# Optimization experiments

Measured on AMD Instinct MI355X. Metric: run time of the kernel, lower is better.

## Reference

```python
import jax, jax.numpy as jnp
import numpy as np

# module hyperparameters (init_kwargs)
WEIGHT = 2e-9
SIGMA_RGB = 0.15   # images in [0,1]; equals canonical 15/255
SIGMA_XY = 100.0
SCALE = 0.5

N, C, K, H, W = 4, 3, 21, 128, 128


def _nearest(x, oh, ow):
    """torch F.interpolate(mode='nearest'): src = floor(dst * in/out)."""
    h, w = x.shape[-2], x.shape[-1]
    iy = jnp.floor(jnp.arange(oh) * (h / oh)).astype(jnp.int32)
    ix = jnp.floor(jnp.arange(ow) * (w / ow)).astype(jnp.int32)
    return x[..., iy[:, None], ix[None, :]]


def _bilinear(x, oh, ow):
    """torch F.interpolate(mode='bilinear', align_corners=False)."""
    h, w = x.shape[-2], x.shape[-1]

    def coords(o, s):
        c = (jnp.arange(o, dtype=jnp.float32) + 0.5) * (s / o) - 0.5
        c = jnp.clip(c, 0.0, s - 1.0)
        c0 = jnp.floor(c).astype(jnp.int32)
        c1 = jnp.minimum(c0 + 1, s - 1)
        return c0, c1, c - c0

    y0, y1, wy = coords(oh, h)
    x0, x1, wx = coords(ow, w)
    wy = wy[:, None]
    wx = wx[None, :]
    v00 = x[..., y0[:, None], x0[None, :]]
    v01 = x[..., y0[:, None], x1[None, :]]
    v10 = x[..., y1[:, None], x0[None, :]]
    v11 = x[..., y1[:, None], x1[None, :]]
    top = v00 * (1.0 - wx) + v01 * wx
    bot = v10 * (1.0 - wx) + v11 * wx
    return top * (1.0 - wy) + bot * wy


def setup_inputs() -> dict:
    key = jax.random.key(0)
    k1, k2 = jax.random.split(key)
    images = jax.random.uniform(k1, (N, C, H, W), jnp.float32)
    segmentations = jax.random.uniform(k2, (N, K, H, W), jnp.float32)
    ROIs = jnp.ones((N, H, W), jnp.float32)
    return {"images": images, "segmentations": segmentations, "ROIs": ROIs}


def reference(images, segmentations, ROIs):
    oh, ow = int(H * SCALE), int(W * SCALE)
    img_s = _nearest(images, oh, ow)           # [N,3,oh,ow]
    seg_s = _bilinear(segmentations, oh, ow)   # [N,K,oh,ow]
    roi_s = _nearest(ROIs, oh, ow)             # [N,oh,ow]
    seg_m = seg_s * roi_s[:, None]             # seg * ROI (per class)
    sxy = SIGMA_XY * SCALE

    # exact dense Gaussian bilateral kernel that the permutohedral lattice
    # (bilateralfilter_batch) approximates: k(i,j) = exp(-|p_i-p_j|^2/(2 sxy^2)
    #                                                  -|I_i-I_j|^2/(2 srgb^2))
    yy, xx = jnp.meshgrid(jnp.arange(oh, dtype=jnp.float32),
                          jnp.arange(ow, dtype=jnp.float32), indexing="ij")
    pos = jnp.stack([xx, yy], 0) / sxy         # [2,oh,ow]

    def per_image(img, seg):
        feat = jnp.concatenate([pos, img / SIGMA_RGB], 0).reshape(5, -1).T  # [P,5]
        sq = jnp.sum(feat * feat, axis=-1)                                  # [P]
        d2 = jnp.maximum(sq[:, None] + sq[None, :] - 2.0 * (feat @ feat.T), 0.0)
        Wk = jnp.exp(-0.5 * d2)                                             # [P,P]
        s = seg.reshape(K, -1)                                              # [K,P]
        AS = s @ Wk                                                         # filtered seg
        return jnp.sum(s * AS)

    vals = jax.vmap(per_image)(img_s, seg_m)   # [N]
    loss = -(jnp.sum(vals)) / N                # densecrf_loss
    return WEIGHT * loss
```

## Files before the change

kernel.cpp:

```cpp
#include <hip/hip_runtime.h>

#define NIMG 4
#define CCH  3
#define KCH  21
#define HIN  128
#define WIN  128
#define OH   64
#define OW   64
#define PPX  (OH*OW)
#define NPIX (NIMG*PPX)

#define PRE2 1.20112241f

#define SEGW  24
#define FEATW 8

#define BLOCK  256
#define JCHUNK 256
#define IBLK   64

#define NSLOT  64

typedef _Float16 half_t;
typedef half_t half8  __attribute__((ext_vector_type(8)));
typedef float  f32x4v __attribute__((ext_vector_type(4)));

#define FEATH_OFF ((size_t)NPIX*SEGW*2)
#define SQF_OFF   (FEATH_OFF + (size_t)NPIX*FEATW*2)
#define SLOT_OFF  (SQF_OFF + (size_t)NPIX*4)

__global__ __launch_bounds__(BLOCK) void crf_prep(const float* __restrict__ img,
                                                  const float* __restrict__ seg,
                                                  const float* __restrict__ roi,
                                                  half_t* __restrict__ segH,
                                                  half_t* __restrict__ featH,
                                                  float* __restrict__ sqF,
                                                  float* __restrict__ slots) {
    int g  = blockIdx.x * BLOCK + threadIdx.x;
    int q  = g >> 14;
    int pl = g & (NPIX - 1);
    int n  = pl >> 12;
    int p  = pl & (PPX - 1);
    int y = p >> 6, x = p & 63;
    int y2 = 2 * y, x2 = 2 * x;

    if (q < SEGW) {
        float v = 0.0f;
        if (q < KCH) {
            const float* s0 = seg + (((size_t)n * KCH + q) * HIN + y2) * WIN + x2;
            float r = roi[((size_t)n * HIN + y2) * WIN + x2];
            v = 0.25f * (s0[0] + s0[1] + s0[WIN] + s0[WIN + 1]) * r;
        }
        segH[(size_t)pl * SEGW + q] = (half_t)v;
    } else if (q == 24) {
        float fx = (float)x * (PRE2 / 50.0f);
        float fy = (float)y * (PRE2 / 50.0f);
        const size_t ib = (((size_t)n * CCH) * HIN + y2) * WIN + x2;
        float fr = img[ib]                         * (PRE2 / 0.15f);
        float fg = img[ib + (size_t)HIN * WIN]     * (PRE2 / 0.15f);
        float fb = img[ib + 2 * (size_t)HIN * WIN] * (PRE2 / 0.15f);
        half_t h0 = (half_t)fx, h1 = (half_t)fy, h2 = (half_t)fr,
               h3 = (half_t)fg, h4 = (half_t)fb;
        half8 fh = {h0, h1, h2, h3, h4, (half_t)0, (half_t)0, (half_t)0};
        *(half8*)(featH + (size_t)pl * FEATW) = fh;
        float a0 = (float)h0, a1 = (float)h1, a2 = (float)h2,
              a3 = (float)h3, a4 = (float)h4;
        sqF[pl] = 0.5f * (a0 * a0 + a1 * a1 + a2 * a2 + a3 * a3 + a4 * a4);
    } else if (q == 25) {
        if (pl < NSLOT) slots[pl * 16] = 0.0f;
    }
}

__global__ __launch_bounds__(BLOCK, 8) void crf_main(const half_t* __restrict__ segH,
                                                     const half_t* __restrict__ featH,
                                                     const float* __restrict__ sqF,
                                                     float* __restrict__ slots) {
    const int bx = blockIdx.x;
    const int n  = blockIdx.y;

    int g = 0;
#pragma unroll
    for (int t = 1; t < 16; ++t) {
        int off = 64 * t - 2 * t * (t - 1);
        if (bx >= off) g = t;
    }
    int rem = bx - (64 * g - 2 * g * (g - 1));
    int c   = 16 - g;
    int iq  = (rem >= c) + (rem >= 2 * c) + (rem >= 3 * c);
    int I   = 4 * g + iq;
    int J   = g + (rem - iq * c);
    const bool diag = (J == (I >> 2));

    const half_t* segN  = segH  + (size_t)n * PPX * SEGW;
    const half_t* featN = featH + (size_t)n * PPX * FEATW;
    const float*  sqN   = sqF   + (size_t)n * PPX;

    __shared__ alignas(16) half_t segJ[JCHUNK * SEGW];
    __shared__ alignas(16) half_t featJ[JCHUNK * FEATW];
    __shared__ alignas(16) half_t zrow[8];
    __shared__ float hJ[JCHUNK];
    __shared__ float wsum[BLOCK / 64];

    const int tid  = threadIdx.x;
    const int lane = tid & 63, wv = tid >> 6;
    const int m = lane & 15, quad = lane >> 4;
    const int ih  = wv >> 1;
    const int jt0 = (wv & 1) * 8;
    const int ib0 = I * 4 + ih * 2;
    const int ib1 = ib0 + 1;
    const int i00 = ib0 << 4;
    const int i01 = i00 + 16;
    const int Jt  = J << 4;
    const int kq  = (quad < 2) ? quad : 2;

    half8 hz = {};

    half8 aseg0  = *(const half8*)(segN  + (size_t)(i00 + m) * SEGW + kq * 8);
    half8 aseg1  = *(const half8*)(segN  + (size_t)(i01 + m) * SEGW + kq * 8);
    half8 afeat0 = *(const half8*)(featN + (size_t)(i00 + m) * FEATW);
    half8 afeat1 = *(const half8*)(featN + (size_t)(i01 + m) * FEATW);
    f32x4v hi0   = *(const f32x4v*)(sqN + i00 + quad * 4);
    f32x4v hi1   = *(const f32x4v*)(sqN + i01 + quad * 4);
    if (quad == 3) { aseg0 = hz; aseg1 = hz; }
    if (quad != 0) { afeat0 = hz; afeat1 = hz; }
    f32x4v nh0 = -hi0, nh1 = -hi1;

    {
        const f32x4v* gsrc = (const f32x4v*)(segN + (size_t)((size_t)Jt << 4) * SEGW);
        f32x4v* ldst = (f32x4v*)segJ;
#pragma unroll
        for (int v = 0; v < 3; ++v) ldst[tid + v * BLOCK] = gsrc[tid + v * BLOCK];
        ((f32x4v*)featJ)[tid] = ((const f32x4v*)(featN + (size_t)((size_t)Jt << 4) * FEATW))[tid];
        hJ[tid] = sqN[(Jt << 4) + tid];
        if (tid < 8) zrow[tid] = (half_t)0;
    }
    __syncthreads();

    const half_t* bsp; int bstep;
    if (quad == 3) { bsp = zrow;                                    bstep = 0; }
    else           { bsp = segJ + (jt0 * 16 + m) * SEGW + quad * 8; bstep = 16 * SEGW; }
    const half_t* bfp; int fstep;
    if (quad == 0) { bfp = featJ + (jt0 * 16 + m) * FEATW;          fstep = 16 * FEATW; }
    else           { bfp = zrow;                                    fstep = 0; }

    float hcv[8];
#pragma unroll
    for (int t = 0; t < 8; ++t) hcv[t] = hJ[(jt0 + t) * 16 + m];

    float racc0 = 0.0f, racc1 = 0.0f;
    const f32x4v zero4 = {0.0f, 0.0f, 0.0f, 0.0f};

#pragma unroll
    for (int t = 0; t < 8; ++t) {
        half8 bseg = *(const half8*)(bsp + t * bstep);
        half8 bft  = *(const half8*)(bfp + t * fstep);
        const float hc = hcv[t];
        const int jb = Jt + jt0 + t;
        const int jg = (jb << 4) + m;

        if (!diag || jb >= ib0) {
            f32x4v c4 = {nh0[0] - hc, nh0[1] - hc, nh0[2] - hc, nh0[3] - hc};
            f32x4v E  = __builtin_amdgcn_mfma_f32_16x16x32_f16(afeat0, bft, c4, 0, 0, 0);
            f32x4v Gs = __builtin_amdgcn_mfma_f32_16x16x32_f16(aseg0, bseg, zero4, 0, 0, 0);
            if (!diag) {
#pragma unroll
                for (int r = 0; r < 4; ++r)
                    racc0 = fmaf(__builtin_amdgcn_exp2f(E[r]), Gs[r], racc0);
            } else if (jb > ib0) {
#pragma unroll
                for (int r = 0; r < 4; ++r)
                    racc0 = fmaf(__builtin_amdgcn_exp2f(E[r] + 1.0f), Gs[r], racc0);
            } else {
#pragma unroll
                for (int r = 0; r < 4; ++r) {
                    int ig = i00 + quad * 4 + r;
                    float sel = (jg > ig) ? 1.0f : ((jg == ig) ? 0.0f : -100000.0f);
                    racc0 = fmaf(__builtin_amdgcn_exp2f(E[r] + sel), Gs[r], racc0);
                }
            }
        }

        if (!diag || jb >= ib1) {
            f32x4v c4 = {nh1[0] - hc, nh1[1] - hc, nh1[2] - hc, nh1[3] - hc};
            f32x4v E  = __builtin_amdgcn_mfma_f32_16x16x32_f16(afeat1, bft, c4, 0, 0, 0);
            f32x4v Gs = __builtin_amdgcn_mfma_f32_16x16x32_f16(aseg1, bseg, zero4, 0, 0, 0);
            if (!diag) {
#pragma unroll
                for (int r = 0; r < 4; ++r)
                    racc1 = fmaf(__builtin_amdgcn_exp2f(E[r]), Gs[r], racc1);
            } else if (jb > ib1) {
#pragma unroll
                for (int r = 0; r < 4; ++r)
                    racc1 = fmaf(__builtin_amdgcn_exp2f(E[r] + 1.0f), Gs[r], racc1);
            } else {
#pragma unroll
                for (int r = 0; r < 4; ++r) {
                    int ig = i01 + quad * 4 + r;
                    float sel = (jg > ig) ? 1.0f : ((jg == ig) ? 0.0f : -100000.0f);
                    racc1 = fmaf(__builtin_amdgcn_exp2f(E[r] + sel), Gs[r], racc1);
                }
            }
        }
    }

    float racc = racc0 + racc1;
#pragma unroll
    for (int off = 32; off > 0; off >>= 1) racc += __shfl_down(racc, off);
    if (lane == 0) wsum[wv] = racc;
    __syncthreads();
    if (tid == 0) {
        float s = wsum[0] + wsum[1] + wsum[2] + wsum[3];
        if (!diag) s *= 2.0f;
        int slot = (bx + 544 * n) & (NSLOT - 1);
        atomicAdd(&slots[slot * 16], s);
    }
}

__global__ __launch_bounds__(64) void crf_final(const float* __restrict__ slots,
                                                float* __restrict__ out) {
    int lane = threadIdx.x;
    float v = slots[lane * 16];
#pragma unroll
    for (int off = 32; off > 0; off >>= 1) v += __shfl_down(v, off);
    if (lane == 0) out[0] = v * (-5.0e-10f);
}

extern "C" void kernel_launch(void* const* d_in, const int* in_sizes, int n_in,
                              void* d_out, int out_size, void* d_ws, size_t ws_size,
                              hipStream_t stream) {
    const float* img = (const float*)d_in[0];
    const float* seg = (const float*)d_in[1];
    const float* roi = (const float*)d_in[2];
    float* out = (float*)d_out;

    char* wsb = (char*)d_ws;
    half_t* segH  = (half_t*)(wsb);
    half_t* featH = (half_t*)(wsb + FEATH_OFF);
    float*  sqF   = (float*)(wsb + SQF_OFF);
    float*  slots = (float*)(wsb + SLOT_OFF);

    crf_prep<<<(NPIX * 26) / BLOCK, BLOCK, 0, stream>>>(img, seg, roi,
                                                        segH, featH, sqF, slots);

    dim3 grid(544, NIMG);
    crf_main<<<grid, BLOCK, 0, stream>>>(segH, featH, sqF, slots);

    crf_final<<<1, 64, 0, stream>>>(slots, out);
}
```

Baseline: 74.53 us.

## Halve J-chunk size to double main-kernel grid and loop prep blocks

Shrinks the J tile per block from 256 to 128 columns and replaces the old triangular index mapping with a simpler one over 32 J-chunks, giving 1056 blocks per image instead of 544. Each block does half the inner MFMA iterations and stages less shared memory. The aim is finer-grained work for better load balance and occupancy across CUs. The prep kernel now runs 416 blocks, each looping over 4 chunks of work, to cut block launch overhead. In exchange, the per-block fixed cost of loading A operands, reducing, and issuing atomics happens twice as often.

```diff
diff --git a/kernel.cpp b/kernel.cpp
--- a/kernel.cpp
+++ b/kernel.cpp
@@ -16,8 +16,11 @@
 #define FEATW 8
 
 #define BLOCK  256
-#define JCHUNK 256
+#define JCHUNK 128
 #define IBLK   64
+
+#define NBLK_IMG 1056
+#define PREPB    416
 
 #define NSLOT  64
 
@@ -36,38 +39,41 @@
                                                   half_t* __restrict__ featH,
                                                   float* __restrict__ sqF,
                                                   float* __restrict__ slots) {
-    int g  = blockIdx.x * BLOCK + threadIdx.x;
-    int q  = g >> 14;
-    int pl = g & (NPIX - 1);
-    int n  = pl >> 12;
-    int p  = pl & (PPX - 1);
-    int y = p >> 6, x = p & 63;
-    int y2 = 2 * y, x2 = 2 * x;
-
-    if (q < SEGW) {
-        float v = 0.0f;
-        if (q < KCH) {
-            const float* s0 = seg + (((size_t)n * KCH + q) * HIN + y2) * WIN + x2;
-            float r = roi[((size_t)n * HIN + y2) * WIN + x2];
-            v = 0.25f * (s0[0] + s0[1] + s0[WIN] + s0[WIN + 1]) * r;
-        }
-        segH[(size_t)pl * SEGW + q] = (half_t)v;
-    } else if (q == 24) {
-        float fx = (float)x * (PRE2 / 50.0f);
-        float fy = (float)y * (PRE2 / 50.0f);
-        const size_t ib = (((size_t)n * CCH) * HIN + y2) * WIN + x2;
-        float fr = img[ib]                         * (PRE2 / 0.15f);
-        float fg = img[ib + (size_t)HIN * WIN]     * (PRE2 / 0.15f);
-        float fb = img[ib + 2 * (size_t)HIN * WIN] * (PRE2 / 0.15f);
-        half_t h0 = (half_t)fx, h1 = (half_t)fy, h2 = (half_t)fr,
-               h3 = (half_t)fg, h4 = (half_t)fb;
-        half8 fh = {h0, h1, h2, h3, h4, (half_t)0, (half_t)0, (half_t)0};
-        *(half8*)(featH + (size_t)pl * FEATW) = fh;
-        float a0 = (float)h0, a1 = (float)h1, a2 = (float)h2,
-              a3 = (float)h3, a4 = (float)h4;
-        sqF[pl] = 0.5f * (a0 * a0 + a1 * a1 + a2 * a2 + a3 * a3 + a4 * a4);
-    } else if (q == 25) {
-        if (pl < NSLOT) slots[pl * 16] = 0.0f;
+#pragma unroll
+    for (int it = 0; it < 4; ++it) {
+        int g  = (blockIdx.x + it * PREPB) * BLOCK + threadIdx.x;
+        int q  = g >> 14;
+        int pl = g & (NPIX - 1);
+        int n  = pl >> 12;
+        int p  = pl & (PPX - 1);
+        int y = p >> 6, x = p & 63;
+        int y2 = 2 * y, x2 = 2 * x;
+
+        if (q < SEGW) {
+            float v = 0.0f;
+            if (q < KCH) {
+                const float* s0 = seg + (((size_t)n * KCH + q) * HIN + y2) * WIN + x2;
+                float r = roi[((size_t)n * HIN + y2) * WIN + x2];
+                v = 0.25f * (s0[0] + s0[1] + s0[WIN] + s0[WIN + 1]) * r;
+            }
+            segH[(size_t)pl * SEGW + q] = (half_t)v;
+        } else if (q == 24) {
+            float fx = (float)x * (PRE2 / 50.0f);
+            float fy = (float)y * (PRE2 / 50.0f);
+            const size_t ib = (((size_t)n * CCH) * HIN + y2) * WIN + x2;
+            float fr = img[ib]                         * (PRE2 / 0.15f);
+            float fg = img[ib + (size_t)HIN * WIN]     * (PRE2 / 0.15f);
+            float fb = img[ib + 2 * (size_t)HIN * WIN] * (PRE2 / 0.15f);
+            half_t h0 = (half_t)fx, h1 = (half_t)fy, h2 = (half_t)fr,
+                   h3 = (half_t)fg, h4 = (half_t)fb;
+            half8 fh = {h0, h1, h2, h3, h4, (half_t)0, (half_t)0, (half_t)0};
+            *(half8*)(featH + (size_t)pl * FEATW) = fh;
+            float a0 = (float)h0, a1 = (float)h1, a2 = (float)h2,
+                  a3 = (float)h3, a4 = (float)h4;
+            sqF[pl] = 0.5f * (a0 * a0 + a1 * a1 + a2 * a2 + a3 * a3 + a4 * a4);
+        } else if (q == 25) {
+            if (pl < NSLOT) slots[pl * 16] = 0.0f;
+        }
     }
 }
 
@@ -78,18 +84,13 @@
     const int bx = blockIdx.x;
     const int n  = blockIdx.y;
 
-    int g = 0;
-#pragma unroll
-    for (int t = 1; t < 16; ++t) {
-        int off = 64 * t - 2 * t * (t - 1);
-        if (bx >= off) g = t;
-    }
-    int rem = bx - (64 * g - 2 * g * (g - 1));
-    int c   = 16 - g;
-    int iq  = (rem >= c) + (rem >= 2 * c) + (rem >= 3 * c);
-    int I   = 4 * g + iq;
-    int J   = g + (rem - iq * c);
-    const bool diag = (J == (I >> 2));
+    int J = 0;
+#pragma unroll
+    for (int t = 1; t < 32; ++t) {
+        if (bx >= t * t + t) J = t;
+    }
+    const int I = bx - (J * J + J);
+    const bool diag = ((I >> 1) == J);
 
     const half_t* segN  = segH  + (size_t)n * PPX * SEGW;
     const half_t* featN = featH + (size_t)n * PPX * FEATW;
@@ -105,12 +106,13 @@
     const int lane = tid & 63, wv = tid >> 6;
     const int m = lane & 15, quad = lane >> 4;
     const int ih  = wv >> 1;
-    const int jt0 = (wv & 1) * 8;
+    const int jt0 = (wv & 1) * 4;
     const int ib0 = I * 4 + ih * 2;
     const int ib1 = ib0 + 1;
     const int i00 = ib0 << 4;
     const int i01 = i00 + 16;
-    const int Jt  = J << 4;
+    const int Jt  = J << 3;
+    const int j0  = J * JCHUNK;
     const int kq  = (quad < 2) ? quad : 2;
 
     half8 hz = {};
@@ -126,12 +128,14 @@
     f32x4v nh0 = -hi0, nh1 = -hi1;
 
     {
-        const f32x4v* gsrc = (const f32x4v*)(segN + (size_t)((size_t)Jt << 4) * SEGW);
+        const f32x4v* gsrc = (const f32x4v*)(segN + (size_t)j0 * SEGW);
         f32x4v* ldst = (f32x4v*)segJ;
-#pragma unroll
-        for (int v = 0; v < 3; ++v) ldst[tid + v * BLOCK] = gsrc[tid + v * BLOCK];
-        ((f32x4v*)featJ)[tid] = ((const f32x4v*)(featN + (size_t)((size_t)Jt << 4) * FEATW))[tid];
-        hJ[tid] = sqN[(Jt << 4) + tid];
+        ldst[tid] = gsrc[tid];
+        if (tid < 128) {
+            ldst[256 + tid] = gsrc[256 + tid];
+            ((f32x4v*)featJ)[tid] = ((const f32x4v*)(featN + (size_t)j0 * FEATW))[tid];
+            hJ[tid] = sqN[j0 + tid];
+        }
         if (tid < 8) zrow[tid] = (half_t)0;
     }
     __syncthreads();
@@ -143,15 +147,15 @@
     if (quad == 0) { bfp = featJ + (jt0 * 16 + m) * FEATW;          fstep = 16 * FEATW; }
     else           { bfp = zrow;                                    fstep = 0; }
 
-    float hcv[8];
-#pragma unroll
-    for (int t = 0; t < 8; ++t) hcv[t] = hJ[(jt0 + t) * 16 + m];
+    float hcv[4];
+#pragma unroll
+    for (int t = 0; t < 4; ++t) hcv[t] = hJ[(jt0 + t) * 16 + m];
 
     float racc0 = 0.0f, racc1 = 0.0f;
     const f32x4v zero4 = {0.0f, 0.0f, 0.0f, 0.0f};
 
 #pragma unroll
-    for (int t = 0; t < 8; ++t) {
+    for (int t = 0; t < 4; ++t) {
         half8 bseg = *(const half8*)(bsp + t * bstep);
         half8 bft  = *(const half8*)(bfp + t * fstep);
         const float hc = hcv[t];
@@ -211,7 +215,7 @@
     if (tid == 0) {
         float s = wsum[0] + wsum[1] + wsum[2] + wsum[3];
         if (!diag) s *= 2.0f;
-        int slot = (bx + 544 * n) & (NSLOT - 1);
+        int slot = (bx + NBLK_IMG * n) & (NSLOT - 1);
         atomicAdd(&slots[slot * 16], s);
     }
 }
@@ -239,10 +243,10 @@
     float*  sqF   = (float*)(wsb + SQF_OFF);
     float*  slots = (float*)(wsb + SLOT_OFF);
 
-    crf_prep<<<(NPIX * 26) / BLOCK, BLOCK, 0, stream>>>(img, seg, roi,
-                                                        segH, featH, sqF, slots);
-
-    dim3 grid(544, NIMG);
+    crf_prep<<<PREPB, BLOCK, 0, stream>>>(img, seg, roi,
+                                          segH, featH, sqF, slots);
+
+    dim3 grid(NBLK_IMG, NIMG);
     crf_main<<<grid, BLOCK, 0, stream>>>(segH, featH, sqF, slots);
 
     crf_final<<<1, 64, 0, stream>>>(slots, out);
```

Measured after the change: 75.19 us. No clear change (+0.9%).
